# Kernel tuning notes

Hardware: AMD Instinct MI355X
Metric: run time of the kernel (lower is better)

Reference implementation:

```python
import jax, jax.numpy as jnp
import numpy as np

N, E = 50000, 800000
IN, HID, OUT = 128, 32, 8


def setup_inputs() -> dict:
    key = jax.random.key(0)
    ks = jax.random.split(key, 20)
    f32 = jnp.float32
    def rn(k, shape, s=0.1):
        return (jax.random.normal(k, shape, dtype=f32) * s)
    return {
        'x': jax.random.normal(ks[0], (N, IN), dtype=f32),
        'edge_index': jax.random.randint(ks[1], (2, E), 0, N, dtype=jnp.int32),
        'edge_attr': jax.random.uniform(ks[2], (E, 1), dtype=f32),
        # layer 1: heads=4, out=HID, concat -> 4*HID channels
        'w1l': rn(ks[3], (IN, 4 * HID)), 'b1l': rn(ks[4], (4 * HID,)),
        'w1r': rn(ks[5], (IN, 4 * HID)), 'b1r': rn(ks[6], (4 * HID,)),
        'w1e': rn(ks[7], (1, 4 * HID)),
        'att1': rn(ks[8], (4, HID)), 'bias1': rn(ks[9], (4 * HID,)),
        # layer 2: heads=2, out=HID, mean over heads -> HID channels
        'w2l': rn(ks[10], (4 * HID, 2 * HID)), 'b2l': rn(ks[11], (2 * HID,)),
        'w2r': rn(ks[12], (4 * HID, 2 * HID)), 'b2r': rn(ks[13], (2 * HID,)),
        'w2e': rn(ks[14], (1, 2 * HID)),
        'att2': rn(ks[15], (2, HID)), 'bias2': rn(ks[16], (HID,)),
        'wc': rn(ks[17], (HID, OUT)), 'bc': rn(ks[18], (OUT,)),
    }


def _add_self_loops(edge_index, edge_attr, n):
    # PyG GATv2Conv adds self-loops; edge feature for loops = mean of edge_attr
    loop = jnp.arange(n, dtype=edge_index.dtype)
    src = jnp.concatenate([edge_index[0], loop])
    dst = jnp.concatenate([edge_index[1], loop])
    mean_attr = jnp.broadcast_to(edge_attr.mean(axis=0), (n, edge_attr.shape[1]))
    ea = jnp.concatenate([edge_attr, mean_attr], axis=0)
    return src, dst, ea


def _gatv2(x, src, dst, eattr, Wl, bl, Wr, br, We, att, bias, heads, out, concat):
    n = x.shape[0]
    xl = (x @ Wl + bl).reshape(n, heads, out)   # source transform (messages)
    xr = (x @ Wr + br).reshape(n, heads, out)   # target transform
    e = (eattr @ We).reshape(-1, heads, out)    # edge embedding
    z = jax.nn.leaky_relu(xl[src] + xr[dst] + e, negative_slope=0.2)  # [Etot,H,D]
    score = jnp.einsum('ehd,hd->eh', z, att)
    # segment softmax over incoming edges of each destination node
    smax = jax.ops.segment_max(score, dst, num_segments=n)
    ex = jnp.exp(score - smax[dst])
    denom = jax.ops.segment_sum(ex, dst, num_segments=n)
    alpha = ex / denom[dst]                     # [Etot,H]
    agg = jax.ops.segment_sum(xl[src] * alpha[..., None], dst, num_segments=n)
    o = agg.reshape(n, heads * out) if concat else agg.mean(axis=1)
    return o + bias


def reference(x, edge_index, edge_attr, w1l, b1l, w1r, b1r, w1e, att1, bias1,
              w2l, b2l, w2r, b2r, w2e, att2, bias2, wc, bc):
    src, dst, ea = _add_self_loops(edge_index, edge_attr, x.shape[0])
    h = _gatv2(x, src, dst, ea, w1l, b1l, w1r, b1r, w1e, att1, bias1, 4, HID, True)
    h = jax.nn.elu(h)
    # dropout p=0.4 is training-only; reference is eval mode (identity)
    h = _gatv2(h, src, dst, ea, w2l, b2l, w2r, b2r, w2e, att2, bias2, 2, HID, False)
    h = jax.nn.elu(h)
    return h @ wc + bc
```

## Files before the change

kernel.cpp:

```cpp
#include <hip/hip_runtime.h>
#include <hip/hip_fp16.h>
#include <math.h>

typedef _Float16 h2_t __attribute__((ext_vector_type(2)));
typedef _Float16 h4_t __attribute__((ext_vector_type(4)));
typedef _Float16 h8_t __attribute__((ext_vector_type(8)));
typedef float f4_t __attribute__((ext_vector_type(4)));
typedef float f8_t __attribute__((ext_vector_type(8)));

#define PRE_BLOCKS 512
#define SB 512
#define NBUK_PAD 800
#define CTB 16

__device__ inline h8_t load8f_to_h8(const float* p) {
    float4 a = *(const float4*)p;
    float4 b = *(const float4*)(p + 4);
    h8_t r;
    r[0] = (_Float16)a.x; r[1] = (_Float16)a.y; r[2] = (_Float16)a.z; r[3] = (_Float16)a.w;
    r[4] = (_Float16)b.x; r[5] = (_Float16)b.y; r[6] = (_Float16)b.z; r[7] = (_Float16)b.w;
    return r;
}

__device__ inline h4_t load4f_to_h4(const float* p) {
    float4 a = *(const float4*)p;
    h4_t r;
    r[0] = (_Float16)a.x; r[1] = (_Float16)a.y; r[2] = (_Float16)a.z; r[3] = (_Float16)a.w;
    return r;
}

__device__ inline float dot8h(h8_t a, h8_t b, float s) {
    s = __builtin_amdgcn_fdot2(__builtin_shufflevector(a, a, 0, 1),
                               __builtin_shufflevector(b, b, 0, 1), s, false);
    s = __builtin_amdgcn_fdot2(__builtin_shufflevector(a, a, 2, 3),
                               __builtin_shufflevector(b, b, 2, 3), s, false);
    s = __builtin_amdgcn_fdot2(__builtin_shufflevector(a, a, 4, 5),
                               __builtin_shufflevector(b, b, 4, 5), s, false);
    s = __builtin_amdgcn_fdot2(__builtin_shufflevector(a, a, 6, 7),
                               __builtin_shufflevector(b, b, 6, 7), s, false);
    return s;
}

__device__ inline float dot4h(h4_t a, h4_t b, float s) {
    s = __builtin_amdgcn_fdot2(__builtin_shufflevector(a, a, 0, 1),
                               __builtin_shufflevector(b, b, 0, 1), s, false);
    s = __builtin_amdgcn_fdot2(__builtin_shufflevector(a, a, 2, 3),
                               __builtin_shufflevector(b, b, 2, 3), s, false);
    return s;
}

__device__ inline float elu1(float v) { return v > 0.f ? v : __expf(v) - 1.f; }

struct MA {
    const float* x;
    const float* eattr;
    const int* ei;
    const float *w1l, *b1l, *w1r, *b1r, *w1e, *att1, *bias1;
    const float *w2l, *b2l, *w2r, *b2r, *w2e, *att2, *bias2;
    const float *wc, *bc;
    float* out;
    _Float16 *xh, *xl1h, *xr1h, *xl2h, *xr2h;
    _Float16 *p1l, *p1r, *p2l, *p2r;
    int *deg, *offb;
    unsigned* parth;
    unsigned* tot;
    unsigned *tstart, *smeanq;
    unsigned* tmp;
    float* part;
    unsigned* edges;
    int N, E, NW, NBK, CE;
    float invE;
};


__device__ inline void phase_packw(const MA& a, int g) {
    const float* W;
    _Float16* P;
    int M, lg;
    if (g < 2048)      { W = a.w1l; P = a.p1l; M = 128; lg = g; }
    else if (g < 4096) { W = a.w1r; P = a.p1r; M = 128; lg = g - 2048; }
    else if (g < 5120) { W = a.w2l; P = a.p2l; M = 64;  lg = g - 4096; }
    else               { W = a.w2r; P = a.p2r; M = 64;  lg = g - 5120; }
    int ln = lg & 63;
    int s = (lg >> 6) & 3;
    int tt = lg >> 8;
    int m = ln & 15, quad = ln >> 4;
    h8_t v;
#pragma unroll
    for (int j = 0; j < 8; ++j)
        v[j] = (_Float16)W[(size_t)(s * 32 + quad * 8 + j) * M + tt * 16 + m];
    *(h8_t*)(P + (size_t)lg * 8) = v;
}

template <int NT>
__device__ inline void phase_mm_tile(const MA& a, const _Float16* X, int rt, int lane,
                                     const _Float16* Pl, const float* bl, _Float16* Yl,
                                     const _Float16* Pr, const float* br, _Float16* Yr) {
    int nrow = lane & 15, quad = lane >> 4;
    int row = rt * 16 + nrow;
    if (row >= a.N) return;
    const _Float16* xp = X + (size_t)row * 128 + quad * 8;
    h8_t bf0 = *(const h8_t*)(xp);
    h8_t bf1 = *(const h8_t*)(xp + 32);
    h8_t bf2 = *(const h8_t*)(xp + 64);
    h8_t bf3 = *(const h8_t*)(xp + 96);
#pragma unroll
    for (int w = 0; w < 2; ++w) {
        const _Float16* P = w ? Pr : Pl;
        const float* bias = w ? br : bl;
        _Float16* Y = w ? Yr : Yl;
#pragma unroll
        for (int t2 = 0; t2 < NT; ++t2) {
            f4_t acc = {0.f, 0.f, 0.f, 0.f};
            const _Float16* pb = P + (size_t)t2 * 2048 + (size_t)lane * 8;
            acc = __builtin_amdgcn_mfma_f32_16x16x32_f16(*(const h8_t*)pb, bf0, acc, 0, 0, 0);
            acc = __builtin_amdgcn_mfma_f32_16x16x32_f16(*(const h8_t*)(pb + 512), bf1, acc, 0, 0, 0);
            acc = __builtin_amdgcn_mfma_f32_16x16x32_f16(*(const h8_t*)(pb + 1024), bf2, acc, 0, 0, 0);
            acc = __builtin_amdgcn_mfma_f32_16x16x32_f16(*(const h8_t*)(pb + 1536), bf3, acc, 0, 0, 0);
            float4 bv = *(const float4*)(bias + t2 * 16 + quad * 4);
            h4_t o;
            o[0] = (_Float16)(acc[0] + bv.x);
            o[1] = (_Float16)(acc[1] + bv.y);
            o[2] = (_Float16)(acc[2] + bv.z);
            o[3] = (_Float16)(acc[3] + bv.w);
            *(h4_t*)(Y + (size_t)row * (NT * 16) + t2 * 16 + quad * 4) = o;
        }
    }
}


__global__ __launch_bounds__(256) void k_pre(MA a) {
    if (blockIdx.x >= PRE_BLOCKS) {
        int g = (blockIdx.x - PRE_BLOCKS) * 256 + threadIdx.x;
        if (g < 6144) phase_packw(a, g);
        return;
    }
    __shared__ unsigned bh[NBUK_PAD];
    __shared__ float sd[4];
    int tx = threadIdx.x;
    for (int j = tx; j < NBUK_PAD; j += 256) bh[j] = 0u;

    int t = blockIdx.x * 256 + tx;
    const int stride = PRE_BLOCKS * 256;
    int nchunk = (a.N * 128) >> 3;
    for (int i = t; i < nchunk; i += stride) {
        h8_t v = load8f_to_h8(a.x + (size_t)i * 8);
        *(h8_t*)(a.xh + (size_t)i * 8) = v;
    }
    float s = 0.f;
    for (int i = t; i < a.E; i += stride) s += a.eattr[i];
    for (int o = 1; o < 64; o <<= 1) s += __shfl_xor(s, o, 64);
    if ((tx & 63) == 0) sd[tx >> 6] = s;
    __syncthreads();
    if (tx == 0) a.part[blockIdx.x] = sd[0] + sd[1] + sd[2] + sd[3];

    int e0 = blockIdx.x * a.CE, e1 = min(e0 + a.CE, a.E);
    for (int e = e0 + tx; e < e1; e += 256)
        atomicAdd(&bh[((unsigned)a.ei[a.E + e]) >> 6], 1u);
    __syncthreads();
    for (int j = tx; j < NBUK_PAD; j += 256)
        a.parth[(size_t)blockIdx.x * NBUK_PAD + j] = bh[j];
}


__global__ __launch_bounds__(512, 1) void k_colscan(MA a) {
    __shared__ unsigned tile[512][CTB + 1];
    int tx = threadIdx.x;
    int b0 = blockIdx.x * CTB;
    unsigned* rp = a.parth + (size_t)tx * NBUK_PAD + b0;
#pragma unroll
    for (int j = 0; j < CTB; ++j) tile[tx][j] = rp[j];
    __syncthreads();

    int c = tx >> 5;
    int g = tx & 31;
    unsigned base = 0;
#pragma unroll
    for (int k = 0; k < 16; ++k) {
        int r = k * 32 + g;
        unsigned orig = tile[r][c];
        unsigned v = orig;
#pragma unroll
        for (int o = 1; o < 32; o <<= 1) {
            unsigned u = __shfl_up(v, o, 32);
            if (g >= o) v += u;
        }
        tile[r][c] = base + (v - orig);
        base += __shfl(v, 31, 32);
    }
    if (g == 0) a.tot[b0 + c] = base;
    __syncthreads();
#pragma unroll
    for (int j = 0; j < CTB; ++j) rp[j] = tile[tx][j];
}


__global__ __launch_bounds__(256) void k_scatter(MA a) {
    int bid = blockIdx.x;
    if (bid < a.NW) {
        int wid = bid * 4 + (threadIdx.x >> 6);
        int ntile = (a.N + 15) / 16;
        if (wid < ntile)
            phase_mm_tile<8>(a, a.xh, wid, threadIdx.x & 63,
                             a.p1l, a.b1l, a.xl1h, a.p1r, a.b1r, a.xr1h);
        return;
    }
    __shared__ unsigned cur[1024];
    __shared__ unsigned wt[4];
    int s = bid - a.NW;
    int tx = threadIdx.x;
    for (int j = tx; j < 1024; j += 256)
        cur[j] = (j < NBUK_PAD) ? a.tot[j] : 0u;
    __syncthreads();
    {
        unsigned x0 = cur[tx * 4], x1 = cur[tx * 4 + 1], x2 = cur[tx * 4 + 2], x3 = cur[tx * 4 + 3];
        unsigned s1 = x0 + x1, s2 = s1 + x2, t = s2 + x3;
        unsigned inc = t;
#pragma unroll
        for (int o = 1; o < 64; o <<= 1) {
            unsigned u = __shfl_up(inc, o, 64);
            if ((tx & 63) >= o) inc += u;
        }
        if ((tx & 63) == 63) wt[tx >> 6] = inc;
        __syncthreads();
        unsigned wb = 0;
#pragma unroll
        for (int k = 0; k < 4; ++k) wb += (k < (tx >> 6)) ? wt[k] : 0u;
        unsigned excl = wb + (inc - t);
        cur[tx * 4]     = excl;
        cur[tx * 4 + 1] = excl + x0;
        cur[tx * 4 + 2] = excl + s1;
        cur[tx * 4 + 3] = excl + s2;
        if (s == 0) {
            if (tx < NBUK_PAD / 4) {
                a.tstart[tx * 4]     = cur[tx * 4];
                a.tstart[tx * 4 + 1] = cur[tx * 4 + 1];
                a.tstart[tx * 4 + 2] = cur[tx * 4 + 2];
                a.tstart[tx * 4 + 3] = cur[tx * 4 + 3];
            }
        }
    }
    __syncthreads();
    if (s == 0) {
        float ss = 0.f;
        for (int j = tx; j < PRE_BLOCKS; j += 256) ss += a.part[j];
        for (int o = 1; o < 64; o <<= 1) ss += __shfl_xor(ss, o, 64);
        __shared__ float rs[4];
        if ((tx & 63) == 0) rs[tx >> 6] = ss;
        __syncthreads();
        if (tx == 0)
            a.smeanq[0] = (unsigned)__float2int_rn((rs[0] + rs[1] + rs[2] + rs[3]) * a.invE * 255.f);
    }
    for (int j = tx; j < NBUK_PAD; j += 256)
        cur[j] += a.parth[(size_t)s * NBUK_PAD + j];
    __syncthreads();
    int e0 = s * a.CE, e1 = min(e0 + a.CE, a.E);
    for (int e = e0 + tx; e < e1; e += 256) {
        int d = a.ei[a.E + e];
        unsigned src = (unsigned)a.ei[e];
        unsigned q = (unsigned)__float2int_rn(a.eattr[e] * 255.f);
        unsigned pos = atomicAdd(&cur[d >> 6], 1u);
        a.tmp[pos] = src | (q << 16) | ((unsigned)(d & 63) << 24);
    }
}


__global__ __launch_bounds__(256) void k_fine(MA a) {
    __shared__ int hist[64];
    __shared__ unsigned cur[64];
    __shared__ unsigned sm;
    int b = blockIdx.x;
    int tx = threadIdx.x;
    int n0 = b << 6;
    int nn = min(64, a.N - n0);
    unsigned ts = a.tstart[b], T = a.tot[b];
    if (tx < 64) hist[tx] = 0;
    if (tx == 0) sm = a.smeanq[0];
    __syncthreads();
    for (unsigned i = tx; i < T; i += 256) {
        unsigned v = a.tmp[ts + i];
        atomicAdd(&hist[(int)(v >> 24)], 1);
    }
    __syncthreads();
    if (tx < 64) {
        int deg1 = hist[tx] + 1;
        int vsc = deg1;
#pragma unroll
        for (int o = 1; o < 64; o <<= 1) {
            int u = __shfl_up(vsc, o, 64);
            if (tx >= o) vsc += u;
        }
        int off = (int)ts + n0 + (vsc - deg1);
        if (tx < nn) {
            a.offb[n0 + tx] = off;
            a.deg[n0 + tx] = deg1;
            a.edges[off] = (unsigned)(n0 + tx) | (sm << 24);
        }
        cur[tx] = (unsigned)(off + 1);
    }
    __syncthreads();
    for (unsigned i = tx; i < T; i += 256) {
        unsigned v = a.tmp[ts + i];
        int loc = (int)(v >> 24);
        unsigned pos = atomicAdd(&cur[loc], 1u);
        a.edges[pos] = (v & 0xFFFFu) | (((v >> 16) & 0xFFu) << 24);
    }
}


__global__ __launch_bounds__(256) void k_n1mm(MA a) {
    __shared__ _Float16 h1s[16 * 128];
    int tid = threadIdx.x;
    int q = tid & 15;
    int nloc = tid >> 4;
    int node = blockIdx.x * 16 + nloc;
    unsigned cb = (unsigned)(q * 16);

    if (node < a.N) {
        h8_t xrv = *(const h8_t*)((const char*)a.xr1h + ((unsigned)node << 8) + cb);
        h8_t wev = load8f_to_h8(a.w1e + q * 8);
        h8_t atv = load8f_to_h8(a.att1 + q * 8);
        const unsigned* ep = a.edges + a.offb[node];
        int deg1 = a.deg[node];
        int last = deg1 - 1;
        const char* xb = (const char*)a.xl1h;

        float l = 0.f;
        f8_t acc = {0.f, 0.f, 0.f, 0.f, 0.f, 0.f, 0.f, 0.f};

        auto GA = [&](unsigned p, bool valid) -> h8_t {
            h8_t r = {};
            if (valid) r = *(const h8_t*)(xb + (((p & 0x00FFFFFFu) << 8) | cb));
            return r;
        };
        auto LOADG = [&](int i, unsigned& p0, unsigned& p1, unsigned& p2, unsigned& p3,
                         h8_t& x0, h8_t& x1, h8_t& x2, h8_t& x3) {
            p0 = ep[i];
            p1 = ep[min(i + 1, last)];
            p2 = ep[min(i + 2, last)];
            p3 = ep[min(i + 3, last)];
            x0 = GA(p0, true);
            x1 = GA(p1, i + 1 < deg1);
            x2 = GA(p2, i + 2 < deg1);
            x3 = GA(p3, i + 3 < deg1);
        };
        auto COMPG = [&](int i, unsigned p0, unsigned p1, unsigned p2, unsigned p3,
                         h8_t x0, h8_t x1, h8_t x2, h8_t x3) {
            float e0 = (float)(p0 >> 24) * (1.f / 255.f);
            float e1 = (float)(p1 >> 24) * (1.f / 255.f);
            float e2 = (float)(p2 >> 24) * (1.f / 255.f);
            float e3 = (float)(p3 >> 24) * (1.f / 255.f);
            h8_t z0 = x0 + xrv + wev * (_Float16)e0;
            z0 = __builtin_elementwise_max(z0, z0 * (_Float16)0.2f);
            float sc0 = dot8h(z0, atv, 0.f);
            h8_t z1 = x1 + xrv + wev * (_Float16)e1;
            z1 = __builtin_elementwise_max(z1, z1 * (_Float16)0.2f);
            float sc1 = dot8h(z1, atv, 0.f);
            h8_t z2 = x2 + xrv + wev * (_Float16)e2;
            z2 = __builtin_elementwise_max(z2, z2 * (_Float16)0.2f);
            float sc2 = dot8h(z2, atv, 0.f);
            h8_t z3 = x3 + xrv + wev * (_Float16)e3;
            z3 = __builtin_elementwise_max(z3, z3 * (_Float16)0.2f);
            float sc3 = dot8h(z3, atv, 0.f);
            sc0 += __shfl_xor(sc0, 1, 64); sc0 += __shfl_xor(sc0, 2, 64);
            sc1 += __shfl_xor(sc1, 1, 64); sc1 += __shfl_xor(sc1, 2, 64);
            sc2 += __shfl_xor(sc2, 1, 64); sc2 += __shfl_xor(sc2, 2, 64);
            sc3 += __shfl_xor(sc3, 1, 64); sc3 += __shfl_xor(sc3, 2, 64);
            float pA = __expf(fminf(sc0, 60.f));
            float pB = (i + 1 < deg1) ? __expf(fminf(sc1, 60.f)) : 0.f;
            float pC = (i + 2 < deg1) ? __expf(fminf(sc2, 60.f)) : 0.f;
            float pD = (i + 3 < deg1) ? __expf(fminf(sc3, 60.f)) : 0.f;
            l += (pA + pB) + (pC + pD);
#pragma unroll
            for (int k = 0; k < 8; ++k)
                acc[k] = fmaf(pA, (float)x0[k],
                         fmaf(pB, (float)x1[k],
                         fmaf(pC, (float)x2[k], fmaf(pD, (float)x3[k], acc[k]))));
        };

        unsigned pa0, pa1, pa2, pa3, pb0, pb1, pb2, pb3;
        h8_t xa0, xa1, xa2, xa3, xb0, xb1, xb2, xb3;
        LOADG(0, pa0, pa1, pa2, pa3, xa0, xa1, xa2, xa3);
        for (int i = 0; i < deg1; i += 8) {
            if (i + 4 < deg1) LOADG(i + 4, pb0, pb1, pb2, pb3, xb0, xb1, xb2, xb3);
            COMPG(i, pa0, pa1, pa2, pa3, xa0, xa1, xa2, xa3);
            if (i + 8 < deg1) LOADG(i + 8, pa0, pa1, pa2, pa3, xa0, xa1, xa2, xa3);
            if (i + 4 < deg1) COMPG(i + 4, pb0, pb1, pb2, pb3, xb0, xb1, xb2, xb3);
        }

        float inv = 1.f / l;
        float4 b0 = *(const float4*)(a.bias1 + q * 8);
        float4 b1 = *(const float4*)(a.bias1 + q * 8 + 4);
        float bb[8] = {b0.x, b0.y, b0.z, b0.w, b1.x, b1.y, b1.z, b1.w};
        h8_t o;
#pragma unroll
        for (int k = 0; k < 8; ++k) o[k] = (_Float16)elu1(fmaf(acc[k], inv, bb[k]));
        *(h8_t*)(h1s + nloc * 128 + q * 8) = o;
    }
    __syncthreads();

    {
        int wv = tid >> 6, lane = tid & 63;
        int nrow = lane & 15, quad = lane >> 4;
        int row = blockIdx.x * 16 + nrow;
        if (row < a.N) {
            const _Float16* xp = h1s + nrow * 128 + quad * 8;
            h8_t bf0 = *(const h8_t*)(xp);
            h8_t bf1 = *(const h8_t*)(xp + 32);
            h8_t bf2 = *(const h8_t*)(xp + 64);
            h8_t bf3 = *(const h8_t*)(xp + 96);
#pragma unroll
            for (int k = 0; k < 2; ++k) {
                int idx = wv * 2 + k;
                int w = idx >> 2, t2 = idx & 3;
                const _Float16* P = w ? a.p2r : a.p2l;
                const float* bias = w ? a.b2r : a.b2l;
                _Float16* Y = w ? a.xr2h : a.xl2h;
                f4_t acc2 = {0.f, 0.f, 0.f, 0.f};
                const _Float16* pb = P + (size_t)t2 * 2048 + (size_t)lane * 8;
                acc2 = __builtin_amdgcn_mfma_f32_16x16x32_f16(*(const h8_t*)pb, bf0, acc2, 0, 0, 0);
                acc2 = __builtin_amdgcn_mfma_f32_16x16x32_f16(*(const h8_t*)(pb + 512), bf1, acc2, 0, 0, 0);
                acc2 = __builtin_amdgcn_mfma_f32_16x16x32_f16(*(const h8_t*)(pb + 1024), bf2, acc2, 0, 0, 0);
                acc2 = __builtin_amdgcn_mfma_f32_16x16x32_f16(*(const h8_t*)(pb + 1536), bf3, acc2, 0, 0, 0);
                float4 bv = *(const float4*)(bias + t2 * 16 + quad * 4);
                h4_t o;
                o[0] = (_Float16)(acc2[0] + bv.x);
                o[1] = (_Float16)(acc2[1] + bv.y);
                o[2] = (_Float16)(acc2[2] + bv.z);
                o[3] = (_Float16)(acc2[3] + bv.w);
                *(h4_t*)(Y + (size_t)row * 64 + t2 * 16 + quad * 4) = o;
            }
        }
    }
}


__global__ __launch_bounds__(256) void k_node2(MA a) {
    __shared__ float h2s[16][33];
    int tid = threadIdx.x;
    int lane = tid & 63;
    int wib = tid >> 6;
    int sub = lane >> 4;
    int r = lane & 15;
    int nloc = wib * 4 + sub;
    int node = blockIdx.x * 16 + nloc;
    int c0 = r * 4;

    if (node < a.N) {
        h4_t xrv = *(const h4_t*)(a.xr2h + (size_t)node * 64 + c0);
        h4_t wev = load4f_to_h4(a.w2e + c0);
        h4_t atv = load4f_to_h4(a.att2 + c0);
        const unsigned* ep = a.edges + a.offb[node];
        int deg1 = a.deg[node];
        int last = deg1 - 1;
        const char* xb = (const char*)a.xl2h;
        unsigned cb = (unsigned)(c0 * 2);
        float l = 0.f;
        float acc[4] = {0.f, 0.f, 0.f, 0.f};
        for (int i = 0; i < deg1; i += 4) {
            unsigned p[4];
            h4_t xv[4];
#pragma unroll
            for (int j = 0; j < 4; ++j) p[j] = ep[min(i + j, last)];
#pragma unroll
            for (int j = 0; j < 4; ++j) {
                xv[j] = h4_t{};
                if (i + j < deg1)
                    xv[j] = *(const h4_t*)(xb + (((p[j] & 0x00FFFFFFu) << 7) | cb));
            }
#pragma unroll
            for (int j = 0; j < 4; ++j) {
                float ea = (float)(p[j] >> 24) * (1.f / 255.f);
                h4_t z = xv[j] + xrv + wev * (_Float16)ea;
                z = __builtin_elementwise_max(z, z * (_Float16)0.2f);
                float sc = dot4h(z, atv, 0.f);
                sc += __shfl_xor(sc, 1, 64);
                sc += __shfl_xor(sc, 2, 64);
                sc += __shfl_xor(sc, 4, 64);
                float pp = (i + j < deg1) ? __expf(fminf(sc, 60.f)) : 0.f;
                l += pp;
#pragma unroll
                for (int k = 0; k < 4; ++k) acc[k] = fmaf(pp, (float)xv[j][k], acc[k]);
            }
        }
        float inv = 1.f / l;
#pragma unroll
        for (int k = 0; k < 4; ++k) {
            float norm = acc[k] * inv;
            float other = __shfl_xor(norm, 8, 64);
            float v = 0.5f * (norm + other);
            if (r < 8) h2s[nloc][c0 + k] = elu1(v + a.bias2[c0 + k]);
        }
    }
    __syncthreads();
    if (tid < 128) {
        int n = tid >> 3, j = tid & 7;
        int gnode = blockIdx.x * 16 + n;
        if (gnode < a.N) {
            float acc = a.bc[j];
#pragma unroll 8
            for (int d = 0; d < 32; ++d) acc = fmaf(h2s[n][d], a.wc[d * 8 + j], acc);
            a.out[(size_t)gnode * 8 + j] = acc;
        }
    }
}


extern "C" void kernel_launch(void* const* d_in, const int* in_sizes, int n_in,
                              void* d_out, int out_size, void* d_ws, size_t ws_size,
                              hipStream_t stream) {
    const int N = in_sizes[0] / 128;
    const int E = in_sizes[2];
    const int tot = E + N;

    char* ws = (char*)d_ws;
    size_t o = 0;
    auto alloc = [&](size_t bytes) -> void* {
        void* p = ws + o;
        o += (bytes + 255) & ~(size_t)255;
        return p;
    };
    MA a;
    a.x     = (const float*)d_in[0];
    a.ei    = (const int*)d_in[1];
    a.eattr = (const float*)d_in[2];
    a.w1l = (const float*)d_in[3];  a.b1l = (const float*)d_in[4];
    a.w1r = (const float*)d_in[5];  a.b1r = (const float*)d_in[6];
    a.w1e = (const float*)d_in[7];  a.att1 = (const float*)d_in[8];
    a.bias1 = (const float*)d_in[9];
    a.w2l = (const float*)d_in[10]; a.b2l = (const float*)d_in[11];
    a.w2r = (const float*)d_in[12]; a.b2r = (const float*)d_in[13];
    a.w2e = (const float*)d_in[14]; a.att2 = (const float*)d_in[15];
    a.bias2 = (const float*)d_in[16];
    a.wc = (const float*)d_in[17];  a.bc = (const float*)d_in[18];
    a.out = (float*)d_out;

    a.xh   = (_Float16*)alloc((size_t)N * 128 * 2);
    a.xl1h = (_Float16*)alloc((size_t)N * 128 * 2);
    a.xr1h = (_Float16*)alloc((size_t)N * 128 * 2);
    a.xl2h = (_Float16*)alloc((size_t)N * 64 * 2);
    a.xr2h = (_Float16*)alloc((size_t)N * 64 * 2);
    a.p1l  = (_Float16*)alloc(128 * 128 * 2);
    a.p1r  = (_Float16*)alloc(128 * 128 * 2);
    a.p2l  = (_Float16*)alloc(128 * 64 * 2);
    a.p2r  = (_Float16*)alloc(128 * 64 * 2);
    a.deg  = (int*)alloc((size_t)N * 4);
    a.offb = (int*)alloc((size_t)N * 4);
    a.parth  = (unsigned*)alloc((size_t)SB * NBUK_PAD * 4);
    a.tot    = (unsigned*)alloc(1024 * 4);
    a.tstart = (unsigned*)alloc(1024 * 4);
    a.smeanq = (unsigned*)alloc(256);
    a.part   = (float*)alloc(PRE_BLOCKS * 4);
    a.tmp    = (unsigned*)alloc((size_t)E * 4);
    a.edges  = (unsigned*)alloc((size_t)tot * 4);
    a.N = N;
    a.E = E;
    a.NW = (N + 63) / 64;
    a.NBK = (N + 63) >> 6;
    a.CE = (E + SB - 1) / SB;
    a.invE = 1.0f / (float)E;

    k_pre<<<PRE_BLOCKS + 24, 256, 0, stream>>>(a);
    k_colscan<<<NBUK_PAD / CTB, 512, 0, stream>>>(a);
    k_scatter<<<a.NW + SB, 256, 0, stream>>>(a);
    k_fine<<<a.NBK, 256, 0, stream>>>(a);
    k_n1mm<<<(N + 15) / 16, 256, 0, stream>>>(a);
    k_node2<<<(N + 15) / 16, 256, 0, stream>>>(a);
}
```

Before: 232.8 us.

## Sort nodes by degree within 64-node buckets and split layer-1 aggregation from matmul

k_fine now builds a permutation that orders the nodes of each 64-node bucket by in-degree. The node kernels process nodes in that order, so the 16-lane groups in a wavefront see similar degrees and suffer less divergence. The fused layer-1 aggregation and MFMA projection kernel is split into k_node1, which writes h1 in fp16 to global memory, and a separate k_mm4 that does the layer-2 projections. This adds a global round-trip for h1, an extra launch and a perm indirection in exchange for balanced per-wave work.

```diff
diff --git a/kernel.cpp b/kernel.cpp
--- a/kernel.cpp
+++ b/kernel.cpp
@@ -59,9 +59,9 @@
     const float *w2l, *b2l, *w2r, *b2r, *w2e, *att2, *bias2;
     const float *wc, *bc;
     float* out;
-    _Float16 *xh, *xl1h, *xr1h, *xl2h, *xr2h;
+    _Float16 *xh, *xl1h, *xr1h, *h1h, *xl2h, *xr2h;
     _Float16 *p1l, *p1r, *p2l, *p2r;
-    int *deg, *offb;
+    int *deg, *offb, *perm;
     unsigned* parth;
     unsigned* tot;
     unsigned *tstart, *smeanq;
@@ -267,6 +267,7 @@
 
 __global__ __launch_bounds__(256) void k_fine(MA a) {
     __shared__ int hist[64];
+    __shared__ int degs[64];
     __shared__ unsigned cur[64];
     __shared__ unsigned sm;
     int b = blockIdx.x;
@@ -284,6 +285,7 @@
     __syncthreads();
     if (tx < 64) {
         int deg1 = hist[tx] + 1;
+        degs[tx] = deg1;
         int vsc = deg1;
 #pragma unroll
         for (int o = 1; o < 64; o <<= 1) {
@@ -299,6 +301,15 @@
         cur[tx] = (unsigned)(off + 1);
     }
     __syncthreads();
+    if (tx < nn) {
+        int d = degs[tx];
+        int rank = 0;
+        for (int j = 0; j < nn; ++j) {
+            int dj = degs[j];
+            rank += (dj < d) || (dj == d && j < tx);
+        }
+        a.perm[n0 + rank] = n0 + tx;
+    }
     for (unsigned i = tx; i < T; i += 256) {
         unsigned v = a.tmp[ts + i];
         int loc = (int)(v >> 24);
@@ -308,130 +319,102 @@
 }
 
 
-__global__ __launch_bounds__(256) void k_n1mm(MA a) {
-    __shared__ _Float16 h1s[16 * 128];
+__global__ __launch_bounds__(256) void k_node1(MA a) {
     int tid = threadIdx.x;
     int q = tid & 15;
-    int nloc = tid >> 4;
-    int node = blockIdx.x * 16 + nloc;
+    int slot = blockIdx.x * 16 + (tid >> 4);
+    if (slot >= a.N) return;
+    int node = a.perm[slot];
     unsigned cb = (unsigned)(q * 16);
 
-    if (node < a.N) {
-        h8_t xrv = *(const h8_t*)((const char*)a.xr1h + ((unsigned)node << 8) + cb);
-        h8_t wev = load8f_to_h8(a.w1e + q * 8);
-        h8_t atv = load8f_to_h8(a.att1 + q * 8);
-        const unsigned* ep = a.edges + a.offb[node];
-        int deg1 = a.deg[node];
-        int last = deg1 - 1;
-        const char* xb = (const char*)a.xl1h;
-
-        float l = 0.f;
-        f8_t acc = {0.f, 0.f, 0.f, 0.f, 0.f, 0.f, 0.f, 0.f};
-
-        auto GA = [&](unsigned p, bool valid) -> h8_t {
-            h8_t r = {};
-            if (valid) r = *(const h8_t*)(xb + (((p & 0x00FFFFFFu) << 8) | cb));
-            return r;
-        };
-        auto LOADG = [&](int i, unsigned& p0, unsigned& p1, unsigned& p2, unsigned& p3,
-                         h8_t& x0, h8_t& x1, h8_t& x2, h8_t& x3) {
-            p0 = ep[i];
-            p1 = ep[min(i + 1, last)];
-            p2 = ep[min(i + 2, last)];
-            p3 = ep[min(i + 3, last)];
-            x0 = GA(p0, true);
-            x1 = GA(p1, i + 1 < deg1);
-            x2 = GA(p2, i + 2 < deg1);
-            x3 = GA(p3, i + 3 < deg1);
-        };
-        auto COMPG = [&](int i, unsigned p0, unsigned p1, unsigned p2, unsigned p3,
-                         h8_t x0, h8_t x1, h8_t x2, h8_t x3) {
-            float e0 = (float)(p0 >> 24) * (1.f / 255.f);
-            float e1 = (float)(p1 >> 24) * (1.f / 255.f);
-            float e2 = (float)(p2 >> 24) * (1.f / 255.f);
-            float e3 = (float)(p3 >> 24) * (1.f / 255.f);
-            h8_t z0 = x0 + xrv + wev * (_Float16)e0;
-            z0 = __builtin_elementwise_max(z0, z0 * (_Float16)0.2f);
-            float sc0 = dot8h(z0, atv, 0.f);
-            h8_t z1 = x1 + xrv + wev * (_Float16)e1;
-            z1 = __builtin_elementwise_max(z1, z1 * (_Float16)0.2f);
-            float sc1 = dot8h(z1, atv, 0.f);
-            h8_t z2 = x2 + xrv + wev * (_Float16)e2;
-            z2 = __builtin_elementwise_max(z2, z2 * (_Float16)0.2f);
-            float sc2 = dot8h(z2, atv, 0.f);
-            h8_t z3 = x3 + xrv + wev * (_Float16)e3;
-            z3 = __builtin_elementwise_max(z3, z3 * (_Float16)0.2f);
-            float sc3 = dot8h(z3, atv, 0.f);
-            sc0 += __shfl_xor(sc0, 1, 64); sc0 += __shfl_xor(sc0, 2, 64);
-            sc1 += __shfl_xor(sc1, 1, 64); sc1 += __shfl_xor(sc1, 2, 64);
-            sc2 += __shfl_xor(sc2, 1, 64); sc2 += __shfl_xor(sc2, 2, 64);
-            sc3 += __shfl_xor(sc3, 1, 64); sc3 += __shfl_xor(sc3, 2, 64);
-            float pA = __expf(fminf(sc0, 60.f));
-            float pB = (i + 1 < deg1) ? __expf(fminf(sc1, 60.f)) : 0.f;
-            float pC = (i + 2 < deg1) ? __expf(fminf(sc2, 60.f)) : 0.f;
-            float pD = (i + 3 < deg1) ? __expf(fminf(sc3, 60.f)) : 0.f;
-            l += (pA + pB) + (pC + pD);
-#pragma unroll
-            for (int k = 0; k < 8; ++k)
-                acc[k] = fmaf(pA, (float)x0[k],
-                         fmaf(pB, (float)x1[k],
-                         fmaf(pC, (float)x2[k], fmaf(pD, (float)x3[k], acc[k]))));
-        };
-
-        unsigned pa0, pa1, pa2, pa3, pb0, pb1, pb2, pb3;
-        h8_t xa0, xa1, xa2, xa3, xb0, xb1, xb2, xb3;
-        LOADG(0, pa0, pa1, pa2, pa3, xa0, xa1, xa2, xa3);
-        for (int i = 0; i < deg1; i += 8) {
-            if (i + 4 < deg1) LOADG(i + 4, pb0, pb1, pb2, pb3, xb0, xb1, xb2, xb3);
-            COMPG(i, pa0, pa1, pa2, pa3, xa0, xa1, xa2, xa3);
-            if (i + 8 < deg1) LOADG(i + 8, pa0, pa1, pa2, pa3, xa0, xa1, xa2, xa3);
-            if (i + 4 < deg1) COMPG(i + 4, pb0, pb1, pb2, pb3, xb0, xb1, xb2, xb3);
-        }
-
-        float inv = 1.f / l;
-        float4 b0 = *(const float4*)(a.bias1 + q * 8);
-        float4 b1 = *(const float4*)(a.bias1 + q * 8 + 4);
-        float bb[8] = {b0.x, b0.y, b0.z, b0.w, b1.x, b1.y, b1.z, b1.w};
-        h8_t o;
-#pragma unroll
-        for (int k = 0; k < 8; ++k) o[k] = (_Float16)elu1(fmaf(acc[k], inv, bb[k]));
-        *(h8_t*)(h1s + nloc * 128 + q * 8) = o;
-    }
-    __syncthreads();
-
-    {
-        int wv = tid >> 6, lane = tid & 63;
-        int nrow = lane & 15, quad = lane >> 4;
-        int row = blockIdx.x * 16 + nrow;
-        if (row < a.N) {
-            const _Float16* xp = h1s + nrow * 128 + quad * 8;
-            h8_t bf0 = *(const h8_t*)(xp);
-            h8_t bf1 = *(const h8_t*)(xp + 32);
-            h8_t bf2 = *(const h8_t*)(xp + 64);
-            h8_t bf3 = *(const h8_t*)(xp + 96);
-#pragma unroll
-            for (int k = 0; k < 2; ++k) {
-                int idx = wv * 2 + k;
-                int w = idx >> 2, t2 = idx & 3;
-                const _Float16* P = w ? a.p2r : a.p2l;
-                const float* bias = w ? a.b2r : a.b2l;
-                _Float16* Y = w ? a.xr2h : a.xl2h;
-                f4_t acc2 = {0.f, 0.f, 0.f, 0.f};
-                const _Float16* pb = P + (size_t)t2 * 2048 + (size_t)lane * 8;
-                acc2 = __builtin_amdgcn_mfma_f32_16x16x32_f16(*(const h8_t*)pb, bf0, acc2, 0, 0, 0);
-                acc2 = __builtin_amdgcn_mfma_f32_16x16x32_f16(*(const h8_t*)(pb + 512), bf1, acc2, 0, 0, 0);
-                acc2 = __builtin_amdgcn_mfma_f32_16x16x32_f16(*(const h8_t*)(pb + 1024), bf2, acc2, 0, 0, 0);
-                acc2 = __builtin_amdgcn_mfma_f32_16x16x32_f16(*(const h8_t*)(pb + 1536), bf3, acc2, 0, 0, 0);
-                float4 bv = *(const float4*)(bias + t2 * 16 + quad * 4);
-                h4_t o;
-                o[0] = (_Float16)(acc2[0] + bv.x);
-                o[1] = (_Float16)(acc2[1] + bv.y);
-                o[2] = (_Float16)(acc2[2] + bv.z);
-                o[3] = (_Float16)(acc2[3] + bv.w);
-                *(h4_t*)(Y + (size_t)row * 64 + t2 * 16 + quad * 4) = o;
-            }
-        }
-    }
+    h8_t xrv = *(const h8_t*)((const char*)a.xr1h + ((unsigned)node << 8) + cb);
+    h8_t wev = load8f_to_h8(a.w1e + q * 8);
+    h8_t atv = load8f_to_h8(a.att1 + q * 8);
+    const unsigned* ep = a.edges + a.offb[node];
+    int deg1 = a.deg[node];
+    int last = deg1 - 1;
+    const char* xb = (const char*)a.xl1h;
+
+    float l = 0.f;
+    f8_t acc = {0.f, 0.f, 0.f, 0.f, 0.f, 0.f, 0.f, 0.f};
+
+    auto GA = [&](unsigned p, bool valid) -> h8_t {
+        h8_t r = {};
+        if (valid) r = *(const h8_t*)(xb + (((p & 0x00FFFFFFu) << 8) | cb));
+        return r;
+    };
+    auto LOADG = [&](int i, unsigned& p0, unsigned& p1, unsigned& p2, unsigned& p3,
+                     h8_t& x0, h8_t& x1, h8_t& x2, h8_t& x3) {
+        p0 = ep[i];
+        p1 = ep[min(i + 1, last)];
+        p2 = ep[min(i + 2, last)];
+        p3 = ep[min(i + 3, last)];
+        x0 = GA(p0, true);
+        x1 = GA(p1, i + 1 < deg1);
+        x2 = GA(p2, i + 2 < deg1);
+        x3 = GA(p3, i + 3 < deg1);
+    };
+    auto COMPG = [&](int i, unsigned p0, unsigned p1, unsigned p2, unsigned p3,
+                     h8_t x0, h8_t x1, h8_t x2, h8_t x3) {
+        float e0 = (float)(p0 >> 24) * (1.f / 255.f);
+        float e1 = (float)(p1 >> 24) * (1.f / 255.f);
+        float e2 = (float)(p2 >> 24) * (1.f / 255.f);
+        float e3 = (float)(p3 >> 24) * (1.f / 255.f);
+        h8_t z0 = x0 + xrv + wev * (_Float16)e0;
+        z0 = __builtin_elementwise_max(z0, z0 * (_Float16)0.2f);
+        float sc0 = dot8h(z0, atv, 0.f);
+        h8_t z1 = x1 + xrv + wev * (_Float16)e1;
+        z1 = __builtin_elementwise_max(z1, z1 * (_Float16)0.2f);
+        float sc1 = dot8h(z1, atv, 0.f);
+        h8_t z2 = x2 + xrv + wev * (_Float16)e2;
+        z2 = __builtin_elementwise_max(z2, z2 * (_Float16)0.2f);
+        float sc2 = dot8h(z2, atv, 0.f);
+        h8_t z3 = x3 + xrv + wev * (_Float16)e3;
+        z3 = __builtin_elementwise_max(z3, z3 * (_Float16)0.2f);
+        float sc3 = dot8h(z3, atv, 0.f);
+        sc0 += __shfl_xor(sc0, 1, 64); sc0 += __shfl_xor(sc0, 2, 64);
+        sc1 += __shfl_xor(sc1, 1, 64); sc1 += __shfl_xor(sc1, 2, 64);
+        sc2 += __shfl_xor(sc2, 1, 64); sc2 += __shfl_xor(sc2, 2, 64);
+        sc3 += __shfl_xor(sc3, 1, 64); sc3 += __shfl_xor(sc3, 2, 64);
+        float pA = __expf(fminf(sc0, 60.f));
+        float pB = (i + 1 < deg1) ? __expf(fminf(sc1, 60.f)) : 0.f;
+        float pC = (i + 2 < deg1) ? __expf(fminf(sc2, 60.f)) : 0.f;
+        float pD = (i + 3 < deg1) ? __expf(fminf(sc3, 60.f)) : 0.f;
+        l += (pA + pB) + (pC + pD);
+#pragma unroll
+        for (int k = 0; k < 8; ++k)
+            acc[k] = fmaf(pA, (float)x0[k],
+                     fmaf(pB, (float)x1[k],
+                     fmaf(pC, (float)x2[k], fmaf(pD, (float)x3[k], acc[k]))));
+    };
+
+    unsigned pa0, pa1, pa2, pa3, pb0, pb1, pb2, pb3;
+    h8_t xa0, xa1, xa2, xa3, xb0, xb1, xb2, xb3;
+    LOADG(0, pa0, pa1, pa2, pa3, xa0, xa1, xa2, xa3);
+    for (int i = 0; i < deg1; i += 8) {
+        if (i + 4 < deg1) LOADG(i + 4, pb0, pb1, pb2, pb3, xb0, xb1, xb2, xb3);
+        COMPG(i, pa0, pa1, pa2, pa3, xa0, xa1, xa2, xa3);
+        if (i + 8 < deg1) LOADG(i + 8, pa0, pa1, pa2, pa3, xa0, xa1, xa2, xa3);
+        if (i + 4 < deg1) COMPG(i + 4, pb0, pb1, pb2, pb3, xb0, xb1, xb2, xb3);
+    }
+
+    float inv = 1.f / l;
+    float4 b0 = *(const float4*)(a.bias1 + q * 8);
+    float4 b1 = *(const float4*)(a.bias1 + q * 8 + 4);
+    float bb[8] = {b0.x, b0.y, b0.z, b0.w, b1.x, b1.y, b1.z, b1.w};
+    h8_t o;
+#pragma unroll
+    for (int k = 0; k < 8; ++k) o[k] = (_Float16)elu1(fmaf(acc[k], inv, bb[k]));
+    *(h8_t*)((char*)a.h1h + ((unsigned)node << 8) + cb) = o;
+}
+
+
+__global__ __launch_bounds__(256) void k_mm4(MA a) {
+    int wid = blockIdx.x * 4 + (threadIdx.x >> 6);
+    int ntile = (a.N + 15) / 16;
+    if (wid >= ntile) return;
+    phase_mm_tile<4>(a, a.h1h, wid, threadIdx.x & 63,
+                     a.p2l, a.b2l, a.xl2h, a.p2r, a.b2r, a.xr2h);
 }
 
 
@@ -443,10 +426,11 @@
     int sub = lane >> 4;
     int r = lane & 15;
     int nloc = wib * 4 + sub;
-    int node = blockIdx.x * 16 + nloc;
+    int slot = blockIdx.x * 16 + nloc;
     int c0 = r * 4;
 
-    if (node < a.N) {
+    if (slot < a.N) {
+        int node = a.perm[slot];
         h4_t xrv = *(const h4_t*)(a.xr2h + (size_t)node * 64 + c0);
         h4_t wev = load4f_to_h4(a.w2e + c0);
         h4_t atv = load4f_to_h4(a.att2 + c0);
@@ -495,8 +479,9 @@
     __syncthreads();
     if (tid < 128) {
         int n = tid >> 3, j = tid & 7;
-        int gnode = blockIdx.x * 16 + n;
-        if (gnode < a.N) {
+        int slot2 = blockIdx.x * 16 + n;
+        if (slot2 < a.N) {
+            int gnode = a.perm[slot2];
             float acc = a.bc[j];
 #pragma unroll 8
             for (int d = 0; d < 32; ++d) acc = fmaf(h2s[n][d], a.wc[d * 8 + j], acc);
@@ -538,6 +523,7 @@
     a.xh   = (_Float16*)alloc((size_t)N * 128 * 2);
     a.xl1h = (_Float16*)alloc((size_t)N * 128 * 2);
     a.xr1h = (_Float16*)alloc((size_t)N * 128 * 2);
+    a.h1h  = (_Float16*)alloc((size_t)N * 128 * 2);
     a.xl2h = (_Float16*)alloc((size_t)N * 64 * 2);
     a.xr2h = (_Float16*)alloc((size_t)N * 64 * 2);
     a.p1l  = (_Float16*)alloc(128 * 128 * 2);
@@ -546,6 +532,7 @@
     a.p2r  = (_Float16*)alloc(128 * 64 * 2);
     a.deg  = (int*)alloc((size_t)N * 4);
     a.offb = (int*)alloc((size_t)N * 4);
+    a.perm = (int*)alloc((size_t)N * 4);
     a.parth  = (unsigned*)alloc((size_t)SB * NBUK_PAD * 4);
     a.tot    = (unsigned*)alloc(1024 * 4);
     a.tstart = (unsigned*)alloc(1024 * 4);
@@ -564,6 +551,7 @@
     k_colscan<<<NBUK_PAD / CTB, 512, 0, stream>>>(a);
     k_scatter<<<a.NW + SB, 256, 0, stream>>>(a);
     k_fine<<<a.NBK, 256, 0, stream>>>(a);
-    k_n1mm<<<(N + 15) / 16, 256, 0, stream>>>(a);
+    k_node1<<<(N + 15) / 16, 256, 0, stream>>>(a);
+    k_mm4<<<(N + 63) / 64, 256, 0, stream>>>(a);
     k_node2<<<(N + 15) / 16, 256, 0, stream>>>(a);
 }
```

Result: slower. 245.0 us (+5.3%).
